# Kernel tuning notes

Measured on AMD Instinct MI355X. Metric: run time of the kernel, lower is better.

## Reference

```python
import jax, jax.numpy as jnp
import numpy as np

N_NODES = 50000
N_EDGES = 800000
D_IN = 128
D_HID = 512
D_OUT = 128


def setup_inputs() -> dict:
    key = jax.random.key(0)
    k1, k2, k3, k4, k5, k6 = jax.random.split(key, 6)
    input_matrix = jax.random.normal(k1, (N_NODES, D_IN), dtype=jnp.float32)
    adjacency_coo_matrix = jax.random.randint(k2, (2, N_EDGES), 0, N_NODES, dtype=jnp.int64)
    # fc net params (torch Linear: y = x @ W.T + b); store W already transposed [D_IN, D_HID]
    lim_fc = 1.0 / np.sqrt(D_IN)
    fc_w = jax.random.uniform(k3, (D_IN, D_HID), dtype=jnp.float32, minval=-lim_fc, maxval=lim_fc)
    fc_b = jax.random.uniform(k4, (D_HID,), dtype=jnp.float32, minval=-lim_fc, maxval=lim_fc)
    # xavier_uniform for [D_IN + D_HID, D_OUT]
    lim_w = np.sqrt(6.0 / (D_IN + D_HID + D_OUT))
    weights_matrix = jax.random.uniform(k5, (D_IN + D_HID, D_OUT), dtype=jnp.float32, minval=-lim_w, maxval=lim_w)
    return {
        "input_matrix": input_matrix,
        "fc_w": fc_w,
        "fc_b": fc_b,
        "weights_matrix": weights_matrix,
        "adjacency_coo_matrix": adjacency_coo_matrix,
    }


def reference(input_matrix, fc_w, fc_b, weights_matrix, adjacency_coo_matrix):
    edge_src, edge_trg = adjacency_coo_matrix[0], adjacency_coo_matrix[1]
    n_nodes = input_matrix.shape[0]
    # gather neighbor features: [E, D_IN]
    neighbors = input_matrix[edge_trg]
    # per-edge MLP + relu: [E, D_HID]
    neighbors_repr = jax.nn.relu(neighbors @ fc_w + fc_b)
    # scatter-max reduce into per-node slots; relu outputs are >= 0, and
    # empty segments map to 0 (matching torch_scatter zero-fill), so clamp at 0
    agg = jax.ops.segment_max(neighbors_repr, edge_src, num_segments=n_nodes)
    agg = jnp.maximum(agg, 0.0)
    concat = jnp.concatenate([input_matrix, agg], axis=1)  # [N, D_IN + D_HID]
    return concat @ weights_matrix  # [N, D_OUT]
```

## Files before the change

### kernel.cpp

```cpp
#include <hip/hip_runtime.h>
#include <hip/hip_bf16.h>

#define N_NODES 50000
#define N_EDGES 800000
#define D_IN 128
#define D_HID 512
#define D_OUT 128
#define CAT_DIM 640
#define CAP 64

typedef __attribute__((ext_vector_type(8))) short short8;
typedef __attribute__((ext_vector_type(4))) float floatx4;

__device__ __forceinline__ unsigned short f2bf(float f) {
    unsigned u = __float_as_uint(f);
    unsigned r = u + 0x7fffu + ((u >> 16) & 1u);
    return (unsigned short)(r >> 16);
}

__device__ __forceinline__ void cvt8(const float* __restrict__ src, unsigned short* o) {
    float4 v0 = *(const float4*)src;
    float4 v1 = *(const float4*)(src + 4);
    o[0] = f2bf(v0.x); o[1] = f2bf(v0.y); o[2] = f2bf(v0.z); o[3] = f2bf(v0.w);
    o[4] = f2bf(v1.x); o[5] = f2bf(v1.y); o[6] = f2bf(v1.z); o[7] = f2bf(v1.w);
}


#define NBKT 196
#define BKT_SHIFT 8
#define CAPB 6144
#define P1_CHUNK 4096
#define P1_BLOCKS 196


#define K0_BLOCKS 256

__global__ __launch_bounds__(256)
void prep_fcw_kernel(const float* __restrict__ fcW, unsigned short* __restrict__ fcwT) {
    int idx = blockIdx.x * 256 + threadIdx.x;
    int k = idx >> 9;
    int n = idx & (D_HID - 1);
    fcwT[n * D_IN + k] = f2bf(fcW[idx]);
}


#define S1_G1_BLOCKS 782
#define S1_WT_BLOCKS 320
#define S1_BLOCKS (P1_BLOCKS + S1_G1_BLOCKS + S1_WT_BLOCKS)
#define G1_PAD 8
#define SM1_BYTES ((64 + 128) * (D_IN + G1_PAD) * 2)

__global__ __launch_bounds__(256)
void sort_gemm1_kernel(const int* __restrict__ adj,
                       int* __restrict__ bucket_cnt, uint2* __restrict__ staging,
                       const float* __restrict__ X,
                       const unsigned short* __restrict__ fcwT,
                       const float* __restrict__ fcb,
                       unsigned short* __restrict__ F,
                       const float* __restrict__ Wm, unsigned short* __restrict__ WT) {
    __shared__ alignas(16) char smem[SM1_BYTES];
    int b = blockIdx.x, tid = threadIdx.x;
    if (b < P1_BLOCKS) {
        uint2* les = (uint2*)smem;
        int* cnt   = (int*)(smem + P1_CHUNK * 8);
        int* woff  = cnt + NBKT;
        for (int i = tid; i < NBKT; i += 256) cnt[i] = 0;
        int v = adj[2 * (tid & 63) + 1];
        int s = (__ballot(v != 0) == 0ULL) ? 2 : 1;
        __syncthreads();
        int e0 = b * P1_CHUNK;
        int ne = N_EDGES - e0; if (ne > P1_CHUNK) ne = P1_CHUNK;
        for (int j = tid; j < ne; j += 256) {
            int e = e0 + j;
            int src, trg;
            if (s == 2) { src = adj[2 * (size_t)e]; trg = adj[2 * ((size_t)N_EDGES + e)]; }
            else        { src = adj[e];             trg = adj[N_EDGES + e]; }
            les[j] = make_uint2((unsigned)src, (unsigned)trg);
            atomicAdd(&cnt[src >> BKT_SHIFT], 1);
        }
        __syncthreads();
        for (int i = tid; i < NBKT; i += 256)
            woff[i] = atomicAdd(&bucket_cnt[i], cnt[i]);
        __syncthreads();
        for (int j = tid; j < ne; j += 256) {
            uint2 et = les[j];
            int bk = (int)(et.x >> BKT_SHIFT);
            int pos = atomicAdd(&woff[bk], 1);
            if (pos < CAPB) staging[(size_t)bk * CAPB + pos] = et;
        }
        return;
    }
    b -= P1_BLOCKS;
    if (b < S1_G1_BLOCKS) {
        typedef unsigned short RowG[D_IN + G1_PAD];
        RowG* As = (RowG*)smem;
        RowG* Bs = (RowG*)(smem + 64 * (D_IN + G1_PAD) * 2);
        int lane = tid & 63, w = tid >> 6;
        int bm = b * 64;
        {
            int r = tid >> 4;
            int c = (tid & 15) * 8;
            #pragma unroll
            for (int p = 0; p < 4; ++p) {
                int row = r + p * 16;
                int gr = bm + row;
                unsigned short o[8] = {0, 0, 0, 0, 0, 0, 0, 0};
                if (gr < N_NODES) cvt8(X + (size_t)gr * D_IN + c, o);
                *(uint4*)(&As[row][c]) = *(const uint4*)o;
            }
        }
        int wm = (w >> 1) * 32, wn = (w & 1) * 64;
        int q = lane >> 4, l16 = lane & 15;
        for (int nc = 0; nc < 4; ++nc) {
            {
                int r = tid >> 4;
                int c = (tid & 15) * 8;
                #pragma unroll
                for (int p = 0; p < 8; ++p) {
                    int row = r + p * 16;
                    *(uint4*)(&Bs[row][c]) =
                        *(const uint4*)(fcwT + (size_t)(nc * 128 + row) * D_IN + c);
                }
            }
            __syncthreads();
            floatx4 acc[2][4] = {};
            #pragma unroll
            for (int ks = 0; ks < 4; ++ks) {
                short8 af[2], bf[4];
                #pragma unroll
                for (int mi = 0; mi < 2; ++mi)
                    af[mi] = *(const short8*)(&As[wm + mi * 16 + l16][ks * 32 + q * 8]);
                #pragma unroll
                for (int ni = 0; ni < 4; ++ni)
                    bf[ni] = *(const short8*)(&Bs[wn + ni * 16 + l16][ks * 32 + q * 8]);
                #pragma unroll
                for (int mi = 0; mi < 2; ++mi)
                    #pragma unroll
                    for (int ni = 0; ni < 4; ++ni)
                        acc[mi][ni] = __builtin_amdgcn_mfma_f32_16x16x32_bf16(af[mi], bf[ni], acc[mi][ni], 0, 0, 0);
            }
            #pragma unroll
            for (int mi = 0; mi < 2; ++mi)
                #pragma unroll
                for (int ni = 0; ni < 4; ++ni)
                    #pragma unroll
                    for (int r = 0; r < 4; ++r) {
                        int row = bm + wm + mi * 16 + q * 4 + r;
                        int col = nc * 128 + wn + ni * 16 + l16;
                        if (row < N_NODES) {
                            float v = fmaxf(acc[mi][ni][r] + fcb[col], 0.0f);
                            F[(size_t)row * D_HID + col] = f2bf(v);
                        }
                    }
            __syncthreads();
        }
        return;
    }
    b -= S1_G1_BLOCKS;
    {
        int idx = b * 256 + tid;
        int k = idx >> 7;
        int n = idx & (D_OUT - 1);
        WT[n * CAT_DIM + k] = f2bf(Wm[idx]);
    }
}


__global__ __launch_bounds__(256)
void sort2_kernel(const int* __restrict__ bucket_cnt, const uint2* __restrict__ staging,
                  int* __restrict__ deg, int* __restrict__ edge_list) {
    __shared__ int ldeg[256];
    int bk = blockIdx.x, tid = threadIdx.x;
    ldeg[tid] = 0;
    __syncthreads();
    int n = bucket_cnt[bk]; if (n > CAPB) n = CAPB;
    int base = bk << BKT_SHIFT;
    const uint2* st = staging + (size_t)bk * CAPB;
    for (int i = tid; i < n; i += 256) {
        uint2 et = st[i];
        int p = atomicAdd(&ldeg[(int)et.x - base], 1);
        if (p < CAP) edge_list[(size_t)et.x * CAP + p] = (int)et.y;
    }
    __syncthreads();
    int src = base + tid;
    if (src < N_NODES) deg[src] = ldeg[tid];
}


__device__ __forceinline__ void fmax_bf16x8(float* acc, const uint4& p) {
    const unsigned* a = (const unsigned*)&p;
    #pragma unroll
    for (int j = 0; j < 4; ++j) {
        unsigned u = a[j];
        acc[2 * j]     = fmaxf(acc[2 * j],     __uint_as_float(u << 16));
        acc[2 * j + 1] = fmaxf(acc[2 * j + 1], __uint_as_float(u & 0xffff0000u));
    }
}

__global__ __launch_bounds__(256)
void aggregate_kernel(const unsigned short* __restrict__ F,
                      const int* __restrict__ deg,
                      const int* __restrict__ edge_list,
                      unsigned short* __restrict__ agg) {
    int gw = (blockIdx.x * 256 + threadIdx.x) >> 6;
    if (gw >= N_NODES) return;
    int lane = threadIdx.x & 63;
    int d = deg[gw];
    d = d < CAP ? d : CAP;
    const int* el = edge_list + gw * CAP;
    float acc[8] = {0.f, 0.f, 0.f, 0.f, 0.f, 0.f, 0.f, 0.f};
    int i = 0;
    for (; i + 2 <= d; i += 2) {
        int t0 = el[i], t1 = el[i + 1];
        uint4 p0 = *(const uint4*)(F + (size_t)t0 * D_HID + lane * 8);
        uint4 p1 = *(const uint4*)(F + (size_t)t1 * D_HID + lane * 8);
        fmax_bf16x8(acc, p0);
        fmax_bf16x8(acc, p1);
    }
    if (i < d) {
        uint4 p0 = *(const uint4*)(F + (size_t)el[i] * D_HID + lane * 8);
        fmax_bf16x8(acc, p0);
    }
    unsigned out[4];
    #pragma unroll
    for (int j = 0; j < 4; ++j) {
        unsigned lo = __float_as_uint(acc[2 * j]) >> 16;
        unsigned hi = __float_as_uint(acc[2 * j + 1]) & 0xffff0000u;
        out[j] = lo | hi;
    }
    *(uint4*)(agg + (size_t)gw * D_HID + lane * 8) = *(uint4*)out;
}


#define GPAD 8
#define GEMM_MT 782

__global__ __launch_bounds__(256)
void gemm2_kernel(const float* __restrict__ X,
                  const unsigned short* __restrict__ agg,
                  const unsigned short* __restrict__ WT,
                  float* __restrict__ out) {
    __shared__ unsigned short As[64][64 + GPAD];
    __shared__ unsigned short Bs[128][64 + GPAD];
    int tid = threadIdx.x;
    int lane = tid & 63, w = tid >> 6;
    int wm = (w >> 1) * 32, wn = (w & 1) * 64;
    int q = lane >> 4, l16 = lane & 15;
    int bm = blockIdx.x * 64;
    floatx4 acc[2][4] = {};
    int ra = tid >> 2;
    int ca = (tid & 3) * 8;
    int rb = tid >> 1;
    int cb = (tid & 1) * 8;

    for (int k0 = 0; k0 < CAT_DIM; k0 += 64) {
        {
            int gr = bm + ra;
            #pragma unroll
            for (int p = 0; p < 2; ++p) {
                int col = k0 + ca + p * 32;
                unsigned short o[8] = {0, 0, 0, 0, 0, 0, 0, 0};
                if (gr < N_NODES) {
                    if (col < D_IN) cvt8(X + (size_t)gr * D_IN + col, o);
                    else *(uint4*)o = *(const uint4*)(agg + (size_t)gr * D_HID + (col - D_IN));
                }
                *(uint4*)(&As[ra][ca + p * 32]) = *(const uint4*)o;
            }
        }
        {
            const unsigned short* bp = WT + (size_t)rb * CAT_DIM + k0 + cb;
            #pragma unroll
            for (int p = 0; p < 4; ++p)
                *(uint4*)(&Bs[rb][cb + p * 16]) = *(const uint4*)(bp + p * 16);
        }
        __syncthreads();
        #pragma unroll
        for (int ks = 0; ks < 2; ++ks) {
            short8 af[2], bf[4];
            #pragma unroll
            for (int mi = 0; mi < 2; ++mi)
                af[mi] = *(const short8*)(&As[wm + mi * 16 + l16][ks * 32 + q * 8]);
            #pragma unroll
            for (int ni = 0; ni < 4; ++ni)
                bf[ni] = *(const short8*)(&Bs[wn + ni * 16 + l16][ks * 32 + q * 8]);
            #pragma unroll
            for (int mi = 0; mi < 2; ++mi)
                #pragma unroll
                for (int ni = 0; ni < 4; ++ni)
                    acc[mi][ni] = __builtin_amdgcn_mfma_f32_16x16x32_bf16(af[mi], bf[ni], acc[mi][ni], 0, 0, 0);
        }
        __syncthreads();
    }

    #pragma unroll
    for (int mi = 0; mi < 2; ++mi)
        #pragma unroll
        for (int ni = 0; ni < 4; ++ni)
            #pragma unroll
            for (int r = 0; r < 4; ++r) {
                int row = bm + wm + mi * 16 + q * 4 + r;
                int col = wn + ni * 16 + l16;
                if (row < N_NODES)
                    out[(size_t)row * D_OUT + col] = acc[mi][ni][r];
            }
}


extern "C" void kernel_launch(void* const* d_in, const int* in_sizes, int n_in,
                              void* d_out, int out_size, void* d_ws, size_t ws_size,
                              hipStream_t stream) {
    const float* X    = (const float*)d_in[0];
    const float* fc_w = (const float*)d_in[1];
    const float* fc_b = (const float*)d_in[2];
    const float* Wm   = (const float*)d_in[3];
    const int*   adj  = (const int*)d_in[4];
    float* outp = (float*)d_out;

    char* ws = (char*)d_ws;
    size_t off = 0;
    auto alloc = [&](size_t bytes) -> void* {
        void* p = ws + off;
        off = (off + bytes + 255) & ~(size_t)255;
        return p;
    };
    unsigned short* agg    = (unsigned short*)alloc((size_t)N_NODES * D_HID * 2);
    unsigned short* F      = (unsigned short*)alloc((size_t)N_NODES * D_HID * 2);
    unsigned short* fcwT   = (unsigned short*)alloc((size_t)D_HID * D_IN * 2);
    unsigned short* WT     = (unsigned short*)alloc((size_t)D_OUT * CAT_DIM * 2);
    int* deg       = (int*)alloc((size_t)N_NODES * 4);
    int* edge_list = (int*)alloc((size_t)N_NODES * CAP * 4);
    int* bucket_cnt = (int*)alloc((size_t)NBKT * 4);
    uint2* staging  = (uint2*)alloc((size_t)NBKT * CAPB * 8);

    hipMemsetAsync(bucket_cnt, 0, (size_t)NBKT * 4, stream);
    prep_fcw_kernel<<<K0_BLOCKS, 256, 0, stream>>>(fc_w, fcwT);
    sort_gemm1_kernel<<<S1_BLOCKS, 256, 0, stream>>>(adj, bucket_cnt, staging,
                                                     X, fcwT, fc_b, F, Wm, WT);
    sort2_kernel<<<NBKT, 256, 0, stream>>>(bucket_cnt, staging, deg, edge_list);
    aggregate_kernel<<<(N_NODES * 64) / 256, 256, 0, stream>>>(F, deg, edge_list, agg);
    gemm2_kernel<<<GEMM_MT, 256, 0, stream>>>(X, agg, WT, outp);
}
```

Before: 280.5 us.

## Split aggregation into two target-half phases with column-sliced blocks for L2 locality

Edge targets are partitioned by whether they fall in the lower or upper half of the node range. Lower-half targets fill the per-node list from the front and upper-half targets from the back, and the two degree counts are packed into one int. Aggregation runs as two kernels, one per half, so that each phase's gather working set of F is smaller and fits better in cache. Each block covers a 64-column slice for 8 nodes, with 8 edges processed in parallel per wave and combined by shuffle reductions. Edge lists shrink to 16-bit indices. The cost is a second launch, a re-read and rewrite of agg, and extra shuffle work.

```diff
diff --git a/kernel.cpp b/kernel.cpp
--- a/kernel.cpp
+++ b/kernel.cpp
@@ -8,6 +8,7 @@
 #define D_OUT 128
 #define CAT_DIM 640
 #define CAP 64
+#define HALF 25000
 
 typedef __attribute__((ext_vector_type(8))) short short8;
 typedef __attribute__((ext_vector_type(4))) float floatx4;
@@ -168,22 +169,29 @@
 
 __global__ __launch_bounds__(256)
 void sort2_kernel(const int* __restrict__ bucket_cnt, const uint2* __restrict__ staging,
-                  int* __restrict__ deg, int* __restrict__ edge_list) {
-    __shared__ int ldeg[256];
+                  int* __restrict__ degp, unsigned short* __restrict__ el16) {
+    __shared__ int lo[256], hi[256];
     int bk = blockIdx.x, tid = threadIdx.x;
-    ldeg[tid] = 0;
+    lo[tid] = 0; hi[tid] = 0;
     __syncthreads();
     int n = bucket_cnt[bk]; if (n > CAPB) n = CAPB;
     int base = bk << BKT_SHIFT;
     const uint2* st = staging + (size_t)bk * CAPB;
     for (int i = tid; i < n; i += 256) {
         uint2 et = st[i];
-        int p = atomicAdd(&ldeg[(int)et.x - base], 1);
-        if (p < CAP) edge_list[(size_t)et.x * CAP + p] = (int)et.y;
+        int r = (int)et.x - base;
+        int t = (int)et.y;
+        if (t < HALF) {
+            int p = atomicAdd(&lo[r], 1);
+            if (p < CAP) el16[(size_t)(base + r) * CAP + p] = (unsigned short)t;
+        } else {
+            int p = atomicAdd(&hi[r], 1);
+            if (p < CAP) el16[(size_t)(base + r) * CAP + (CAP - 1 - p)] = (unsigned short)t;
+        }
     }
     __syncthreads();
     int src = base + tid;
-    if (src < N_NODES) deg[src] = ldeg[tid];
+    if (src < N_NODES) degp[src] = lo[tid] | (hi[tid] << 16);
 }
 
 
@@ -197,38 +205,64 @@
     }
 }
 
-__global__ __launch_bounds__(256)
-void aggregate_kernel(const unsigned short* __restrict__ F,
-                      const int* __restrict__ deg,
-                      const int* __restrict__ edge_list,
-                      unsigned short* __restrict__ agg) {
-    int gw = (blockIdx.x * 256 + threadIdx.x) >> 6;
-    if (gw >= N_NODES) return;
-    int lane = threadIdx.x & 63;
-    int d = deg[gw];
-    d = d < CAP ? d : CAP;
-    const int* el = edge_list + gw * CAP;
-    float acc[8] = {0.f, 0.f, 0.f, 0.f, 0.f, 0.f, 0.f, 0.f};
-    int i = 0;
-    for (; i + 2 <= d; i += 2) {
-        int t0 = el[i], t1 = el[i + 1];
-        uint4 p0 = *(const uint4*)(F + (size_t)t0 * D_HID + lane * 8);
-        uint4 p1 = *(const uint4*)(F + (size_t)t1 * D_HID + lane * 8);
-        fmax_bf16x8(acc, p0);
-        fmax_bf16x8(acc, p1);
-    }
-    if (i < d) {
-        uint4 p0 = *(const uint4*)(F + (size_t)el[i] * D_HID + lane * 8);
-        fmax_bf16x8(acc, p0);
-    }
-    unsigned out[4];
+template<int H>
+__global__ __launch_bounds__(256)
+void aggregate_phase(const unsigned short* __restrict__ F,
+                     const int* __restrict__ degp,
+                     const unsigned short* __restrict__ el16,
+                     unsigned short* __restrict__ agg) {
+    int tid = threadIdx.x;
+    int lane = tid & 63, w = tid >> 6;
+    int s = blockIdx.x & 7;
+    int g = blockIdx.x >> 3;
+    int sub = lane >> 3;
+    int ch  = lane & 7;
+    const unsigned short* Fs = F + s * 64 + ch * 8;
     #pragma unroll
-    for (int j = 0; j < 4; ++j) {
-        unsigned lo = __float_as_uint(acc[2 * j]) >> 16;
-        unsigned hi = __float_as_uint(acc[2 * j + 1]) & 0xffff0000u;
-        out[j] = lo | hi;
-    }
-    *(uint4*)(agg + (size_t)gw * D_HID + lane * 8) = *(uint4*)out;
+    for (int k = 0; k < 2; ++k) {
+        int n = g * 8 + w * 2 + k;
+        int dp = degp[n];
+        int d = H ? (dp >> 16) : (dp & 0xffff);
+        d = d < CAP ? d : CAP;
+        float acc[8];
+        if (H) {
+            uint4 a0 = *(const uint4*)(agg + (size_t)n * D_HID + s * 64 + ch * 8);
+            const unsigned* au = (const unsigned*)&a0;
+            #pragma unroll
+            for (int j = 0; j < 4; ++j) {
+                acc[2 * j]     = __uint_as_float(au[j] << 16);
+                acc[2 * j + 1] = __uint_as_float(au[j] & 0xffff0000u);
+            }
+        } else {
+            #pragma unroll
+            for (int j = 0; j < 8; ++j) acc[j] = 0.0f;
+        }
+        for (int i = 0; i < d; i += 8) {
+            int e = i + sub;
+            if (e < d) {
+                int slot = H ? (CAP - 1 - e) : e;
+                int t = el16[(size_t)n * CAP + slot];
+                uint4 p = *(const uint4*)(Fs + (size_t)t * D_HID);
+                fmax_bf16x8(acc, p);
+            }
+        }
+        #pragma unroll
+        for (int j = 0; j < 8; ++j) {
+            acc[j] = fmaxf(acc[j], __shfl_xor(acc[j], 8, 64));
+            acc[j] = fmaxf(acc[j], __shfl_xor(acc[j], 16, 64));
+            acc[j] = fmaxf(acc[j], __shfl_xor(acc[j], 32, 64));
+        }
+        if (sub == 0) {
+            unsigned o[4];
+            #pragma unroll
+            for (int j = 0; j < 4; ++j) {
+                unsigned lov = __float_as_uint(acc[2 * j]) >> 16;
+                unsigned hiv = __float_as_uint(acc[2 * j + 1]) & 0xffff0000u;
+                o[j] = lov | hiv;
+            }
+            *(uint4*)(agg + (size_t)n * D_HID + s * 64 + ch * 8) = *(uint4*)o;
+        }
+    }
 }
 
 
@@ -327,8 +361,8 @@
     unsigned short* F      = (unsigned short*)alloc((size_t)N_NODES * D_HID * 2);
     unsigned short* fcwT   = (unsigned short*)alloc((size_t)D_HID * D_IN * 2);
     unsigned short* WT     = (unsigned short*)alloc((size_t)D_OUT * CAT_DIM * 2);
-    int* deg       = (int*)alloc((size_t)N_NODES * 4);
-    int* edge_list = (int*)alloc((size_t)N_NODES * CAP * 4);
+    int* degp      = (int*)alloc((size_t)N_NODES * 4);
+    unsigned short* el16 = (unsigned short*)alloc((size_t)N_NODES * CAP * 2);
     int* bucket_cnt = (int*)alloc((size_t)NBKT * 4);
     uint2* staging  = (uint2*)alloc((size_t)NBKT * CAPB * 8);
 
@@ -336,7 +370,8 @@
     prep_fcw_kernel<<<K0_BLOCKS, 256, 0, stream>>>(fc_w, fcwT);
     sort_gemm1_kernel<<<S1_BLOCKS, 256, 0, stream>>>(adj, bucket_cnt, staging,
                                                      X, fcwT, fc_b, F, Wm, WT);
-    sort2_kernel<<<NBKT, 256, 0, stream>>>(bucket_cnt, staging, deg, edge_list);
-    aggregate_kernel<<<(N_NODES * 64) / 256, 256, 0, stream>>>(F, deg, edge_list, agg);
+    sort2_kernel<<<NBKT, 256, 0, stream>>>(bucket_cnt, staging, degp, el16);
+    aggregate_phase<0><<<(N_NODES / 8) * 8, 256, 0, stream>>>(F, degp, el16, agg);
+    aggregate_phase<1><<<(N_NODES / 8) * 8, 256, 0, stream>>>(F, degp, el16, agg);
     gemm2_kernel<<<GEMM_MT, 256, 0, stream>>>(X, agg, WT, outp);
 }
```

Measured after the change: 417.5 us. 48.8% more time.
